# Performance work log

Hardware: AMD Instinct MI355X
Metric: run time of the kernel (lower is better)

The kernel has to match this reference:

```python
import jax, jax.numpy as jnp
import numpy as np

B, S, D, H = 4, 2048, 1024, 16
HD = D // H  # head_size = 64


def setup_inputs() -> dict:
    key = jax.random.key(0)
    ks = jax.random.split(key, 8)
    scale = 1.0 / np.sqrt(D)
    return {
        "q": jax.random.normal(ks[0], (B, S, D), dtype=jnp.float32),
        "k": jax.random.normal(ks[1], (B, S, D), dtype=jnp.float32),
        "v": jax.random.normal(ks[2], (B, S, D), dtype=jnp.float32),
        "mask": jnp.ones((B, 1, S, S), dtype=jnp.int32),
        "W_q": jax.random.normal(ks[3], (D, D), dtype=jnp.float32) * scale,
        "W_k": jax.random.normal(ks[4], (D, D), dtype=jnp.float32) * scale,
        "W_v": jax.random.normal(ks[5], (D, D), dtype=jnp.float32) * scale,
        "W_o": jax.random.normal(ks[6], (D, D), dtype=jnp.float32) * scale,
    }


def reference(q, k, v, mask, W_q, W_k, W_v, W_o):
    # Linear projections (nn.Linear with bias=False: x @ W.T; here W stored as (D_out, D_in))
    query = q @ W_q.T  # (B,S,D)
    key_ = k @ W_k.T
    value = v @ W_v.T
    # split heads -> (B,H,S,hd)
    query = query.reshape(B, S, H, HD).transpose(0, 2, 1, 3)
    key_ = key_.reshape(B, S, H, HD).transpose(0, 2, 1, 3)
    value = value.reshape(B, S, H, HD).transpose(0, 2, 1, 3)
    # scaled dot-product attention, materializing full (B,H,S,S) scores as original does
    att = jnp.einsum('bhqd,bhkd->bhqk', query, key_) * (HD ** -0.5)
    att = jnp.where(mask == 0, -jnp.inf, att)
    att = jax.nn.softmax(att, axis=-1)
    y = jnp.einsum('bhqk,bhkd->bhqd', att, value)
    y = y.transpose(0, 2, 1, 3).reshape(B, S, D)
    return y @ W_o.T
```

## Files before the change

kernel.cpp:

```cpp
#include <hip/hip_runtime.h>
#include <stdint.h>

#define B_ 4
#define S_ 2048
#define D_ 1024
#define H_ 16
#define HD_ 64
#define K_ 1024
#define N_ 1024

typedef __attribute__((ext_vector_type(8))) short short8;
typedef __attribute__((ext_vector_type(4))) float f32x4;

#define MFMA16(a,b,c) __builtin_amdgcn_mfma_f32_16x16x32_bf16((a),(b),(c),0,0,0)

__device__ __forceinline__ unsigned short f2bf(float f) {
  union { float f; uint32_t u; } v; v.f = f;
  uint32_t u = v.u;
  u += 0x7fffu + ((u >> 16) & 1u);
  return (unsigned short)(u >> 16);
}
__device__ __forceinline__ uint32_t packbf(float a, float b) {
  return (uint32_t)f2bf(a) | ((uint32_t)f2bf(b) << 16);
}

typedef __attribute__((address_space(1))) const uint32_t gbl_u32;
typedef __attribute__((address_space(3))) uint32_t lds_u32;

__device__ __forceinline__ void gload_lds16(const void* g, void* l) {
  __builtin_amdgcn_global_load_lds((gbl_u32*)g, (lds_u32*)l, 16, 0, 0);
}

__global__ __launch_bounds__(256)
void cvt_qkv(const float* __restrict__ q, const float* __restrict__ k, const float* __restrict__ v,
             unsigned short* __restrict__ qo, unsigned short* __restrict__ ko, unsigned short* __restrict__ vo)
{
  const float* s; unsigned short* d;
  if (blockIdx.z == 0)      { s = q; d = qo; }
  else if (blockIdx.z == 1) { s = k; d = ko; }
  else                      { s = v; d = vo; }
  const size_t i = ((size_t)blockIdx.x * 256 + threadIdx.x) * 4;
  const float4 f = *(const float4*)(s + i);
  ushort4 o;
  o.x = f2bf(f.x); o.y = f2bf(f.y); o.z = f2bf(f.z); o.w = f2bf(f.w);
  *(ushort4*)(d + i) = o;
}

__global__ __launch_bounds__(256)
void cvt_w(const float* __restrict__ a, const float* __restrict__ b,
           const float* __restrict__ c, const float* __restrict__ dd,
           unsigned short* __restrict__ ao, unsigned short* __restrict__ bo,
           unsigned short* __restrict__ co, unsigned short* __restrict__ eo)
{
  const float* s; unsigned short* d;
  switch (blockIdx.z) {
    case 0:  s = a;  d = ao; break;
    case 1:  s = b;  d = bo; break;
    case 2:  s = c;  d = co; break;
    default: s = dd; d = eo; break;
  }
  const size_t i = ((size_t)blockIdx.x * 256 + threadIdx.x) * 4;
  const float4 f = *(const float4*)(s + i);
  ushort4 o;
  o.x = f2bf(f.x); o.y = f2bf(f.y); o.z = f2bf(f.z); o.w = f2bf(f.w);
  *(ushort4*)(d + i) = o;
}

template<int EPI>
__global__ __launch_bounds__(256)
void gemm_bt(const unsigned short* __restrict__ A, const unsigned short* __restrict__ Bt,
             float* __restrict__ Cf, unsigned short* __restrict__ Cb, float scale)
{
  __shared__ unsigned short As[128 * 64];
  __shared__ unsigned short Bs[128 * 64];
  const int tid  = threadIdx.x;
  const int lane = tid & 63, wave = tid >> 6;
  const int r15 = lane & 15, g = lane >> 4;
  const int sw = (r15 & 7) << 4;
  const int m0 = blockIdx.y * 128, n0 = blockIdx.x * 128;
  const int wm = (wave >> 1) * 64, wn = (wave & 1) * 64;
  f32x4 acc[4][4] = {};
  const char* AsB = (const char*)As;
  const char* BsB = (const char*)Bs;

  for (int kt = 0; kt < K_; kt += 64) {
    #pragma unroll
    for (int i = 0; i < 4; ++i) {
      const int off  = i * 4096 + tid * 16;
      const int row  = off >> 7;
      const int srcb = (off & 127) ^ ((row & 7) << 4);
      const int col  = kt + (srcb >> 1);
      gload_lds16(A  + (size_t)(m0 + row) * K_ + col, (char*)As + off);
      gload_lds16(Bt + (size_t)(n0 + row) * K_ + col, (char*)Bs + off);
    }
    __syncthreads();
    #pragma unroll
    for (int kc = 0; kc < 2; ++kc) {
      short8 af[4], bfr[4];
      #pragma unroll
      for (int mf = 0; mf < 4; ++mf)
        af[mf] = *(const short8*)(AsB + (wm + mf*16 + r15) * 128 + ((kc*64 + g*16) ^ sw));
      #pragma unroll
      for (int nf = 0; nf < 4; ++nf)
        bfr[nf] = *(const short8*)(BsB + (wn + nf*16 + r15) * 128 + ((kc*64 + g*16) ^ sw));
      #pragma unroll
      for (int mf = 0; mf < 4; ++mf)
        #pragma unroll
        for (int nf = 0; nf < 4; ++nf)
          acc[mf][nf] = MFMA16(af[mf], bfr[nf], acc[mf][nf]);
    }
    __syncthreads();
  }

  #pragma unroll
  for (int mf = 0; mf < 4; ++mf) {
    #pragma unroll
    for (int nf = 0; nf < 4; ++nf) {
      const int col   = n0 + wn + nf*16 + r15;
      const int rbase = m0 + wm + mf*16 + g*4;
      if constexpr (EPI == 0) {
        #pragma unroll
        for (int r = 0; r < 4; ++r)
          Cf[(size_t)(rbase + r) * N_ + col] = acc[mf][nf][r] * scale;
      } else if constexpr (EPI == 1) {
        const int hh = col >> 6, dd = col & 63;
        #pragma unroll
        for (int r = 0; r < 4; ++r) {
          const int row = rbase + r;
          const int bb = row >> 11, ss = row & (S_ - 1);
          Cb[(((size_t)(bb * H_ + hh)) * S_ + ss) * HD_ + dd] = f2bf(acc[mf][nf][r] * scale);
        }
      } else {
        const int hh = col >> 6, dd = col & 63;
        const int bb = rbase >> 11, ss = rbase & (S_ - 1);
        ushort4 o;
        o.x = f2bf(acc[mf][nf][0] * scale);
        o.y = f2bf(acc[mf][nf][1] * scale);
        o.z = f2bf(acc[mf][nf][2] * scale);
        o.w = f2bf(acc[mf][nf][3] * scale);
        *(ushort4*)&Cb[(((size_t)(bb * H_ + hh)) * HD_ + dd) * S_ + ss] = o;
      }
    }
  }
}

__global__ __launch_bounds__(256)
void attn(const unsigned short* __restrict__ Qp, const unsigned short* __restrict__ Kp,
          const unsigned short* __restrict__ Vt, unsigned short* __restrict__ Y)
{
  __shared__ unsigned short Ks[64 * 64];
  __shared__ unsigned short Vs[64 * 64];
  const int tid  = threadIdx.x;
  const int lane = tid & 63, wave = tid >> 6;
  const int r15 = lane & 15, g = lane >> 4;
  const int sw = (r15 & 7) << 4;
  const int bh = blockIdx.y, bb = bh >> 4, hh = bh & 15;
  const int q0 = blockIdx.x * 64 + wave * 16;
  const size_t qkbase = (size_t)bh * (S_ * HD_);
  const size_t vtbase = (size_t)bh * (HD_ * S_);
  const f32x4 zero4 = {0.f, 0.f, 0.f, 0.f};
  const short8 qf0 = *(const short8*)&Qp[qkbase + (size_t)(q0 + r15) * HD_ + g*8];
  const short8 qf1 = *(const short8*)&Qp[qkbase + (size_t)(q0 + r15) * HD_ + 32 + g*8];
  f32x4 y0 = zero4, y1 = zero4, y2 = zero4, y3 = zero4;
  float mrun = -__builtin_inff(), lrun = 0.f;
  const char* KsB = (const char*)Ks;
  const char* VsB = (const char*)Vs;

  for (int k0 = 0; k0 < S_; k0 += 64) {
    #pragma unroll
    for (int i = 0; i < 2; ++i) {
      const int off  = i * 4096 + tid * 16;
      const int row  = off >> 7;
      const int srcb = (off & 127) ^ ((row & 7) << 4);
      gload_lds16(&Kp[qkbase + (size_t)(k0 + row) * HD_ + (srcb >> 1)], (char*)Ks + off);
      gload_lds16(&Vt[vtbase + (size_t)row * S_ + k0 + (srcb >> 1)],    (char*)Vs + off);
    }
    __syncthreads();

    f32x4 sc[2][2];
    #pragma unroll
    for (int c = 0; c < 2; ++c) {
      #pragma unroll
      for (int kf = 0; kf < 2; ++kf) {
        const int row = c*32 + kf*16 + r15;
        const short8 ka0 = *(const short8*)(KsB + row*128 + ((g*16) ^ sw));
        const short8 ka1 = *(const short8*)(KsB + row*128 + ((64 + g*16) ^ sw));
        f32x4 s = MFMA16(ka0, qf0, zero4);
        s = MFMA16(ka1, qf1, s);
        sc[c][kf] = s;
      }
    }

    float mx = -__builtin_inff();
    #pragma unroll
    for (int c = 0; c < 2; ++c)
      #pragma unroll
      for (int kf = 0; kf < 2; ++kf)
        #pragma unroll
        for (int r = 0; r < 4; ++r)
          mx = fmaxf(mx, sc[c][kf][r]);
    mx = fmaxf(mx, __shfl_xor(mx, 16));
    mx = fmaxf(mx, __shfl_xor(mx, 32));
    const float mnew  = fmaxf(mrun, mx);
    const float alpha = __expf(mrun - mnew);
    mrun = mnew;
    f32x4 p[2][2];
    float rs = 0.f;
    #pragma unroll
    for (int c = 0; c < 2; ++c)
      #pragma unroll
      for (int kf = 0; kf < 2; ++kf)
        #pragma unroll
        for (int r = 0; r < 4; ++r) {
          const float e = __expf(sc[c][kf][r] - mnew);
          p[c][kf][r] = e;
          rs += e;
        }
    rs += __shfl_xor(rs, 16);
    rs += __shfl_xor(rs, 32);
    lrun = lrun * alpha + rs;
    y0 *= alpha; y1 *= alpha; y2 *= alpha; y3 *= alpha;

    const int src0 = r15 + 16 * ((2*g) & 3);
    const bool hi = g >= 2;
    #pragma unroll
    for (int c = 0; c < 2; ++c) {
      const uint32_t a01 = packbf(p[c][0][0], p[c][0][1]);
      const uint32_t a23 = packbf(p[c][0][2], p[c][0][3]);
      const uint32_t b01 = packbf(p[c][1][0], p[c][1][1]);
      const uint32_t b23 = packbf(p[c][1][2], p[c][1][3]);
      const uint32_t t0a = (uint32_t)__shfl((int)a01, src0);
      const uint32_t t1a = (uint32_t)__shfl((int)a23, src0);
      const uint32_t t2a = (uint32_t)__shfl((int)a01, src0 + 16);
      const uint32_t t3a = (uint32_t)__shfl((int)a23, src0 + 16);
      const uint32_t t0b = (uint32_t)__shfl((int)b01, src0);
      const uint32_t t1b = (uint32_t)__shfl((int)b23, src0);
      const uint32_t t2b = (uint32_t)__shfl((int)b01, src0 + 16);
      const uint32_t t3b = (uint32_t)__shfl((int)b23, src0 + 16);
      union { uint32_t u[4]; short8 v8; } pf;
      pf.u[0] = hi ? t0b : t0a;
      pf.u[1] = hi ? t1b : t1a;
      pf.u[2] = hi ? t2b : t2a;
      pf.u[3] = hi ? t3b : t3a;
      const int kb = c * 64;
      short8 va;
      va = *(const short8*)(VsB + (0*16 + r15)*128 + ((kb + g*16) ^ sw)); y0 = MFMA16(va, pf.v8, y0);
      va = *(const short8*)(VsB + (1*16 + r15)*128 + ((kb + g*16) ^ sw)); y1 = MFMA16(va, pf.v8, y1);
      va = *(const short8*)(VsB + (2*16 + r15)*128 + ((kb + g*16) ^ sw)); y2 = MFMA16(va, pf.v8, y2);
      va = *(const short8*)(VsB + (3*16 + r15)*128 + ((kb + g*16) ^ sw)); y3 = MFMA16(va, pf.v8, y3);
    }
    __syncthreads();
  }

  const float inv = 1.0f / lrun;
  const int qq = q0 + r15;
  f32x4 yy[4] = {y0, y1, y2, y3};
  #pragma unroll
  for (int n = 0; n < 4; ++n) {
    ushort4 o;
    o.x = f2bf(yy[n][0] * inv);
    o.y = f2bf(yy[n][1] * inv);
    o.z = f2bf(yy[n][2] * inv);
    o.w = f2bf(yy[n][3] * inv);
    const int d = n*16 + g*4;
    *(ushort4*)&Y[((size_t)(bb * S_ + qq)) * D_ + hh * HD_ + d] = o;
  }
}

extern "C" void kernel_launch(void* const* d_in, const int* in_sizes, int n_in,
                              void* d_out, int out_size, void* d_ws, size_t ws_size,
                              hipStream_t stream)
{
  const float* q  = (const float*)d_in[0];
  const float* k  = (const float*)d_in[1];
  const float* v  = (const float*)d_in[2];
  const float* Wq = (const float*)d_in[4];
  const float* Wk = (const float*)d_in[5];
  const float* Wv = (const float*)d_in[6];
  const float* Wo = (const float*)d_in[7];
  float* out = (float*)d_out;
  char* ws = (char*)d_ws;

  unsigned short* qb  = (unsigned short*)(ws + 0);
  unsigned short* kb  = (unsigned short*)(ws + (16u << 20));
  unsigned short* vb  = (unsigned short*)(ws + (32u << 20));
  unsigned short* Wqb = (unsigned short*)(ws + (48u << 20));
  unsigned short* Wkb = (unsigned short*)(ws + (50u << 20));
  unsigned short* Wvb = (unsigned short*)(ws + (52u << 20));
  unsigned short* Wob = (unsigned short*)(ws + (54u << 20));
  unsigned short* Qp  = (unsigned short*)(ws + (56u << 20));
  unsigned short* Kp  = (unsigned short*)(ws + (72u << 20));
  unsigned short* Vt  = (unsigned short*)(ws + (88u << 20));
  unsigned short* Yb  = qb;

  dim3 blk(256, 1, 1);
  cvt_qkv<<<dim3(8192, 1, 3), blk, 0, stream>>>(q, k, v, qb, kb, vb);
  cvt_w  <<<dim3(1024, 1, 4), blk, 0, stream>>>(Wq, Wk, Wv, Wo, Wqb, Wkb, Wvb, Wob);
  gemm_bt<1><<<dim3(8, 64, 1), blk, 0, stream>>>(qb, Wqb, nullptr, Qp, 0.125f);
  gemm_bt<1><<<dim3(8, 64, 1), blk, 0, stream>>>(kb, Wkb, nullptr, Kp, 1.0f);
  gemm_bt<2><<<dim3(8, 64, 1), blk, 0, stream>>>(vb, Wvb, nullptr, Vt, 1.0f);
  attn<<<dim3(32, 64, 1), blk, 0, stream>>>(Qp, Kp, Vt, Yb);
  gemm_bt<0><<<dim3(8, 64, 1), blk, 0, stream>>>(Yb, Wob, out, nullptr, 1.0f);

  (void)in_sizes; (void)n_in; (void)out_size; (void)ws_size;
}
```

Before: 435.6 us.

## Rewrite attention with 32x32 MFMA tiles, exp2 softmax, and lazy rescaling

The attention kernel moves from 16x16x32 to 32x32x16 bf16 MFMA. Each wave now handles 32 queries, so each block covers 128 queries and the grid is halved, which doubles K/V tile reuse per LDS load. Softmax uses exp2, with log2(e) folded into the Q projection scale. It also skips the running-max rescale unless the max grows by more than 8. The P repacking uses hardware cvt_pk_bf16 and permlane32_swap instead of many shuffles, and s_setprio is raised around the MFMA sections. The trade-offs are higher register pressure and fewer blocks (lower occupancy), and the deferred rescale relies on exp2 headroom in fp32.

```diff
diff --git a/kernel.cpp b/kernel.cpp
--- a/kernel.cpp
+++ b/kernel.cpp
@@ -11,8 +11,10 @@
 
 typedef __attribute__((ext_vector_type(8))) short short8;
 typedef __attribute__((ext_vector_type(4))) float f32x4;
+typedef __attribute__((ext_vector_type(16))) float f32x16;
 
 #define MFMA16(a,b,c) __builtin_amdgcn_mfma_f32_16x16x32_bf16((a),(b),(c),0,0,0)
+#define MFMA32(a,b,c) __builtin_amdgcn_mfma_f32_32x32x16_bf16((a),(b),(c),0,0,0)
 
 __device__ __forceinline__ unsigned short f2bf(float f) {
   union { float f; uint32_t u; } v; v.f = f;
@@ -20,8 +22,29 @@
   u += 0x7fffu + ((u >> 16) & 1u);
   return (unsigned short)(u >> 16);
 }
-__device__ __forceinline__ uint32_t packbf(float a, float b) {
-  return (uint32_t)f2bf(a) | ((uint32_t)f2bf(b) << 16);
+
+__device__ __forceinline__ uint32_t cvtpk(float lo, float hi) {
+  uint32_t r;
+  asm("v_cvt_pk_bf16_f32 %0, %1, %2" : "=v"(r) : "v"(lo), "v"(hi));
+  return r;
+}
+
+__device__ __forceinline__ void pl32swap(uint32_t &a, uint32_t &b) {
+#if __has_builtin(__builtin_amdgcn_permlane32_swap)
+  typedef __attribute__((ext_vector_type(2))) int i32x2;
+  i32x2 r = __builtin_amdgcn_permlane32_swap((int)a, (int)b, false, false);
+  a = (uint32_t)r[0]; b = (uint32_t)r[1];
+#else
+  asm volatile("s_nop 1\n\tv_permlane32_swap_b32 %0, %1\n\ts_nop 1" : "+v"(a), "+v"(b));
+#endif
+}
+
+__device__ __forceinline__ float fexp2(float x) {
+#if __has_builtin(__builtin_amdgcn_exp2f)
+  return __builtin_amdgcn_exp2f(x);
+#else
+  return exp2f(x);
+#endif
 }
 
 typedef __attribute__((address_space(1))) const uint32_t gbl_u32;
@@ -152,19 +175,23 @@
   __shared__ unsigned short Vs[64 * 64];
   const int tid  = threadIdx.x;
   const int lane = tid & 63, wave = tid >> 6;
-  const int r15 = lane & 15, g = lane >> 4;
-  const int sw = (r15 & 7) << 4;
+  const int l31 = lane & 31, h = lane >> 5;
+  const int sw = (l31 & 7) << 4;
   const int bh = blockIdx.y, bb = bh >> 4, hh = bh & 15;
-  const int q0 = blockIdx.x * 64 + wave * 16;
+  const int q0w = blockIdx.x * 128 + wave * 32;
   const size_t qkbase = (size_t)bh * (S_ * HD_);
   const size_t vtbase = (size_t)bh * (HD_ * S_);
-  const f32x4 zero4 = {0.f, 0.f, 0.f, 0.f};
-  const short8 qf0 = *(const short8*)&Qp[qkbase + (size_t)(q0 + r15) * HD_ + g*8];
-  const short8 qf1 = *(const short8*)&Qp[qkbase + (size_t)(q0 + r15) * HD_ + 32 + g*8];
-  f32x4 y0 = zero4, y1 = zero4, y2 = zero4, y3 = zero4;
-  float mrun = -__builtin_inff(), lrun = 0.f;
   const char* KsB = (const char*)Ks;
   const char* VsB = (const char*)Vs;
+
+  short8 qf[4];
+  #pragma unroll
+  for (int sl = 0; sl < 4; ++sl)
+    qf[sl] = *(const short8*)&Qp[qkbase + (size_t)(q0w + l31) * HD_ + sl*16 + h*8];
+
+  f32x16 yA = {0,0,0,0,0,0,0,0,0,0,0,0,0,0,0,0};
+  f32x16 yB = {0,0,0,0,0,0,0,0,0,0,0,0,0,0,0,0};
+  float mrun = -__builtin_inff(), lrun = 0.f;
 
   for (int k0 = 0; k0 < S_; k0 += 64) {
     #pragma unroll
@@ -177,93 +204,95 @@
     }
     __syncthreads();
 
-    f32x4 sc[2][2];
-    #pragma unroll
-    for (int c = 0; c < 2; ++c) {
+    f32x16 sc0 = {0,0,0,0,0,0,0,0,0,0,0,0,0,0,0,0};
+    f32x16 sc1 = {0,0,0,0,0,0,0,0,0,0,0,0,0,0,0,0};
+    __builtin_amdgcn_s_setprio(1);
+    #pragma unroll
+    for (int sl = 0; sl < 4; ++sl) {
+      const int colb = (sl*32 + h*16) ^ sw;
+      const short8 ka0 = *(const short8*)(KsB + l31*128 + colb);
+      const short8 ka1 = *(const short8*)(KsB + (32 + l31)*128 + colb);
+      sc0 = MFMA32(ka0, qf[sl], sc0);
+      sc1 = MFMA32(ka1, qf[sl], sc1);
+    }
+    __builtin_amdgcn_s_setprio(0);
+
+    float t[16];
+    #pragma unroll
+    for (int r = 0; r < 16; ++r) t[r] = fmaxf(sc0[r], sc1[r]);
+    #pragma unroll
+    for (int r = 0; r < 8; ++r) t[r] = fmaxf(t[r], t[r+8]);
+    #pragma unroll
+    for (int r = 0; r < 4; ++r) t[r] = fmaxf(t[r], t[r+4]);
+    t[0] = fmaxf(fmaxf(t[0], t[1]), fmaxf(t[2], t[3]));
+    float pmax = fmaxf(t[0], __shfl_xor(t[0], 32));
+
+    if (!__all(pmax <= mrun + 8.0f)) {
+      const float mnew  = fmaxf(mrun, pmax);
+      const float alpha = fexp2(mrun - mnew);
+      mrun = mnew;
       #pragma unroll
-      for (int kf = 0; kf < 2; ++kf) {
-        const int row = c*32 + kf*16 + r15;
-        const short8 ka0 = *(const short8*)(KsB + row*128 + ((g*16) ^ sw));
-        const short8 ka1 = *(const short8*)(KsB + row*128 + ((64 + g*16) ^ sw));
-        f32x4 s = MFMA16(ka0, qf0, zero4);
-        s = MFMA16(ka1, qf1, s);
-        sc[c][kf] = s;
-      }
-    }
-
-    float mx = -__builtin_inff();
-    #pragma unroll
-    for (int c = 0; c < 2; ++c)
-      #pragma unroll
-      for (int kf = 0; kf < 2; ++kf)
-        #pragma unroll
-        for (int r = 0; r < 4; ++r)
-          mx = fmaxf(mx, sc[c][kf][r]);
-    mx = fmaxf(mx, __shfl_xor(mx, 16));
-    mx = fmaxf(mx, __shfl_xor(mx, 32));
-    const float mnew  = fmaxf(mrun, mx);
-    const float alpha = __expf(mrun - mnew);
-    mrun = mnew;
-    f32x4 p[2][2];
-    float rs = 0.f;
-    #pragma unroll
-    for (int c = 0; c < 2; ++c)
-      #pragma unroll
-      for (int kf = 0; kf < 2; ++kf)
-        #pragma unroll
-        for (int r = 0; r < 4; ++r) {
-          const float e = __expf(sc[c][kf][r] - mnew);
-          p[c][kf][r] = e;
-          rs += e;
-        }
-    rs += __shfl_xor(rs, 16);
+      for (int r = 0; r < 16; ++r) { yA[r] *= alpha; yB[r] *= alpha; }
+      lrun *= alpha;
+    }
+    #pragma unroll
+    for (int r = 0; r < 16; ++r) {
+      sc0[r] = fexp2(sc0[r] - mrun);
+      sc1[r] = fexp2(sc1[r] - mrun);
+    }
+    float s[16];
+    #pragma unroll
+    for (int r = 0; r < 16; ++r) s[r] = sc0[r] + sc1[r];
+    #pragma unroll
+    for (int r = 0; r < 8; ++r) s[r] += s[r+8];
+    #pragma unroll
+    for (int r = 0; r < 4; ++r) s[r] += s[r+4];
+    float rs = (s[0] + s[1]) + (s[2] + s[3]);
     rs += __shfl_xor(rs, 32);
-    lrun = lrun * alpha + rs;
-    y0 *= alpha; y1 *= alpha; y2 *= alpha; y3 *= alpha;
-
-    const int src0 = r15 + 16 * ((2*g) & 3);
-    const bool hi = g >= 2;
-    #pragma unroll
-    for (int c = 0; c < 2; ++c) {
-      const uint32_t a01 = packbf(p[c][0][0], p[c][0][1]);
-      const uint32_t a23 = packbf(p[c][0][2], p[c][0][3]);
-      const uint32_t b01 = packbf(p[c][1][0], p[c][1][1]);
-      const uint32_t b23 = packbf(p[c][1][2], p[c][1][3]);
-      const uint32_t t0a = (uint32_t)__shfl((int)a01, src0);
-      const uint32_t t1a = (uint32_t)__shfl((int)a23, src0);
-      const uint32_t t2a = (uint32_t)__shfl((int)a01, src0 + 16);
-      const uint32_t t3a = (uint32_t)__shfl((int)a23, src0 + 16);
-      const uint32_t t0b = (uint32_t)__shfl((int)b01, src0);
-      const uint32_t t1b = (uint32_t)__shfl((int)b23, src0);
-      const uint32_t t2b = (uint32_t)__shfl((int)b01, src0 + 16);
-      const uint32_t t3b = (uint32_t)__shfl((int)b23, src0 + 16);
-      union { uint32_t u[4]; short8 v8; } pf;
-      pf.u[0] = hi ? t0b : t0a;
-      pf.u[1] = hi ? t1b : t1a;
-      pf.u[2] = hi ? t2b : t2a;
-      pf.u[3] = hi ? t3b : t3a;
-      const int kb = c * 64;
-      short8 va;
-      va = *(const short8*)(VsB + (0*16 + r15)*128 + ((kb + g*16) ^ sw)); y0 = MFMA16(va, pf.v8, y0);
-      va = *(const short8*)(VsB + (1*16 + r15)*128 + ((kb + g*16) ^ sw)); y1 = MFMA16(va, pf.v8, y1);
-      va = *(const short8*)(VsB + (2*16 + r15)*128 + ((kb + g*16) ^ sw)); y2 = MFMA16(va, pf.v8, y2);
-      va = *(const short8*)(VsB + (3*16 + r15)*128 + ((kb + g*16) ^ sw)); y3 = MFMA16(va, pf.v8, y3);
-    }
+    lrun += rs;
+
+    uint32_t pf[4][4];
+    #pragma unroll
+    for (int ks = 0; ks < 4; ++ks) {
+      const f32x16& sv = (ks < 2) ? sc0 : sc1;
+      const int rb = (ks & 1) * 8;
+      uint32_t x0 = cvtpk(sv[rb+0], sv[rb+1]);
+      uint32_t x1 = cvtpk(sv[rb+2], sv[rb+3]);
+      uint32_t y0 = cvtpk(sv[rb+4], sv[rb+5]);
+      uint32_t y1 = cvtpk(sv[rb+6], sv[rb+7]);
+      pl32swap(x0, y0);
+      pl32swap(x1, y1);
+      pf[ks][0] = x0; pf[ks][1] = x1; pf[ks][2] = y0; pf[ks][3] = y1;
+    }
+
+    __builtin_amdgcn_s_setprio(1);
+    #pragma unroll
+    for (int ks = 0; ks < 4; ++ks) {
+      union { uint32_t u[4]; short8 v; } pu;
+      pu.u[0] = pf[ks][0]; pu.u[1] = pf[ks][1]; pu.u[2] = pf[ks][2]; pu.u[3] = pf[ks][3];
+      const int colb = (ks*32 + h*16) ^ sw;
+      const short8 va0 = *(const short8*)(VsB + l31*128 + colb);
+      const short8 va1 = *(const short8*)(VsB + (32 + l31)*128 + colb);
+      yA = MFMA32(va0, pu.v, yA);
+      yB = MFMA32(va1, pu.v, yB);
+    }
+    __builtin_amdgcn_s_setprio(0);
     __syncthreads();
   }
 
   const float inv = 1.0f / lrun;
-  const int qq = q0 + r15;
-  f32x4 yy[4] = {y0, y1, y2, y3};
+  const int qg = q0w + l31;
+  unsigned short* Yrow = &Y[((size_t)(bb * S_ + qg)) * D_ + hh * HD_];
   #pragma unroll
-  for (int n = 0; n < 4; ++n) {
-    ushort4 o;
-    o.x = f2bf(yy[n][0] * inv);
-    o.y = f2bf(yy[n][1] * inv);
-    o.z = f2bf(yy[n][2] * inv);
-    o.w = f2bf(yy[n][3] * inv);
-    const int d = n*16 + g*4;
-    *(ushort4*)&Y[((size_t)(bb * S_ + qq)) * D_ + hh * HD_ + d] = o;
+  for (int tq = 0; tq < 4; ++tq) {
+    ushort4 oa, ob;
+    oa.x = f2bf(yA[4*tq+0] * inv); oa.y = f2bf(yA[4*tq+1] * inv);
+    oa.z = f2bf(yA[4*tq+2] * inv); oa.w = f2bf(yA[4*tq+3] * inv);
+    ob.x = f2bf(yB[4*tq+0] * inv); ob.y = f2bf(yB[4*tq+1] * inv);
+    ob.z = f2bf(yB[4*tq+2] * inv); ob.w = f2bf(yB[4*tq+3] * inv);
+    const int d = 8*tq + 4*h;
+    *(ushort4*)&Yrow[d]      = oa;
+    *(ushort4*)&Yrow[32 + d] = ob;
   }
 }
 
@@ -296,10 +325,10 @@
   dim3 blk(256, 1, 1);
   cvt_qkv<<<dim3(8192, 1, 3), blk, 0, stream>>>(q, k, v, qb, kb, vb);
   cvt_w  <<<dim3(1024, 1, 4), blk, 0, stream>>>(Wq, Wk, Wv, Wo, Wqb, Wkb, Wvb, Wob);
-  gemm_bt<1><<<dim3(8, 64, 1), blk, 0, stream>>>(qb, Wqb, nullptr, Qp, 0.125f);
+  gemm_bt<1><<<dim3(8, 64, 1), blk, 0, stream>>>(qb, Wqb, nullptr, Qp, 0.18033688f);
   gemm_bt<1><<<dim3(8, 64, 1), blk, 0, stream>>>(kb, Wkb, nullptr, Kp, 1.0f);
   gemm_bt<2><<<dim3(8, 64, 1), blk, 0, stream>>>(vb, Wvb, nullptr, Vt, 1.0f);
-  attn<<<dim3(32, 64, 1), blk, 0, stream>>>(Qp, Kp, Vt, Yb);
+  attn<<<dim3(16, 64, 1), blk, 0, stream>>>(Qp, Kp, Vt, Yb);
   gemm_bt<0><<<dim3(8, 64, 1), blk, 0, stream>>>(Yb, Wob, out, nullptr, 1.0f);
 
   (void)in_sizes; (void)n_in; (void)out_size; (void)ws_size;
```

Result: faster. 388.3 us (-10.9%).
